# Optimization experiments

Hardware: AMD Instinct MI355X
Metric: run time of the kernel (lower is better)

The kernel has to match this reference:

```python
import jax, jax.numpy as jnp
import numpy as np
import math

D_MODEL = 1024
N_HEAD = 16


def setup_inputs() -> dict:
    key = jax.random.key(0)
    ks = jax.random.split(key, 11)
    B, S, D = 2, 2048, D_MODEL
    s = 1.0 / math.sqrt(D)
    return {
        "q": jax.random.normal(ks[0], (B, S, D), dtype=jnp.float32),
        "k": jax.random.normal(ks[1], (B, S, D), dtype=jnp.float32),
        "v": jax.random.normal(ks[2], (B, S, D), dtype=jnp.float32),
        "w_q": jax.random.normal(ks[3], (D, D), dtype=jnp.float32) * s,
        "b_q": jnp.zeros((D,), dtype=jnp.float32),
        "w_k": jax.random.normal(ks[4], (D, D), dtype=jnp.float32) * s,
        "b_k": jnp.zeros((D,), dtype=jnp.float32),
        "w_v": jax.random.normal(ks[5], (D, D), dtype=jnp.float32) * s,
        "b_v": jnp.zeros((D,), dtype=jnp.float32),
        "w_out": jax.random.normal(ks[6], (D, D), dtype=jnp.float32) * s,
        "b_out": jnp.zeros((D,), dtype=jnp.float32),
    }


def _split_heads(x, n_head):
    B, S, D = x.shape
    return x.reshape(B, S, n_head, D // n_head).transpose(0, 2, 1, 3)  # [B,H,S,dk]


def reference(q, k, v, w_q, b_q, w_k, b_k, w_v, b_v, w_out, b_out):
    # Linear projections (weights stored as [in, out])
    qh = _split_heads(q @ w_q + b_q, N_HEAD)
    kh = _split_heads(k @ w_k + b_k, N_HEAD)
    vh = _split_heads(v @ w_v + b_v, N_HEAD)
    d_k = qh.shape[-1]
    scores = jnp.einsum("bhqd,bhkd->bhqk", qh, kh) / jnp.sqrt(jnp.float32(d_k))
    attn = jax.nn.softmax(scores, axis=-1)
    context = jnp.einsum("bhqk,bhkd->bhqd", attn, vh)  # [B,H,S,dk]
    B, H, S, dk = context.shape
    context = context.transpose(0, 2, 1, 3).reshape(B, S, H * dk)
    return context @ w_out + b_out
```

## Files before the change

kernel.cpp:

```cpp
#include <hip/hip_runtime.h>
#include <hip/hip_bf16.h>


typedef __bf16 bf16x8 __attribute__((ext_vector_type(8)));
typedef float  f32x4  __attribute__((ext_vector_type(4)));

#define DEVI __device__ __forceinline__
#define SWZ(row, cb) ((cb) ^ (((row) & 7) << 4))

#define GLOAD16(gsrc, ldst)                                                    \
    __builtin_amdgcn_global_load_lds(                                          \
        (const __attribute__((address_space(1))) unsigned int*)(gsrc),         \
        (__attribute__((address_space(3))) unsigned int*)(ldst), 16, 0, 0)

#define BAR()        asm volatile("s_barrier" ::: "memory")
#define WAIT_LGKM0() asm volatile("s_waitcnt lgkmcnt(0)" ::: "memory")
#define WAIT_VM0()   asm volatile("s_waitcnt vmcnt(0)" ::: "memory")
#define WAIT_VM4()   asm volatile("s_waitcnt vmcnt(4)" ::: "memory")

static DEVI unsigned short f2bf(float f) {
    __hip_bfloat16 h = __float2bfloat16(f);
    return __builtin_bit_cast(unsigned short, h);
}
static DEVI unsigned int pack2(float a, float b) {
    return (unsigned int)f2bf(a) | ((unsigned int)f2bf(b) << 16);
}
static DEVI bf16x8 ldsRead(const char* p) {
    return __builtin_bit_cast(bf16x8, *(const uint4*)p);
}

__global__ __launch_bounds__(256) void wtrans_kernel(
    const float* w0, const float* w1, const float* w2, const float* w3,
    unsigned short* t0, unsigned short* t1, unsigned short* t2, unsigned short* t3)
{
    __shared__ unsigned short tile[64][80];
    const int z = blockIdx.z;
    const float* w = (z == 0) ? w0 : (z == 1) ? w1 : (z == 2) ? w2 : w3;
    unsigned short* wt = (z == 0) ? t0 : (z == 1) ? t1 : (z == 2) ? t2 : t3;
    const int n0 = blockIdx.x * 64, k0 = blockIdx.y * 64;
    const int t = threadIdx.x;
#pragma unroll
    for (int i = 0; i < 4; i++) {
        int chunk = t + i * 256;
        int row = chunk >> 4, c4 = chunk & 15;
        float4 v = *(const float4*)(w + (size_t)(k0 + row) * 1024 + n0 + c4 * 4);
        tile[c4 * 4 + 0][row] = f2bf(v.x);
        tile[c4 * 4 + 1][row] = f2bf(v.y);
        tile[c4 * 4 + 2][row] = f2bf(v.z);
        tile[c4 * 4 + 3][row] = f2bf(v.w);
    }
    __syncthreads();
#pragma unroll
    for (int i = 0; i < 2; i++) {
        int idx = t + i * 256;
        int row = idx >> 3, ch = idx & 7;
        uint4 vv = *(const uint4*)(&tile[row][ch * 8]);
        *(uint4*)(wt + (size_t)(n0 + row) * 1024 + k0 + ch * 8) = vv;
    }
}

__global__ __launch_bounds__(256, 3) void gemm_proj_kernel(
    const float* x0, const float* x1, const float* x2,
    const unsigned short* wt0, const unsigned short* wt1, const unsigned short* wt2,
    const float* b0, const float* b1, const float* b2,
    unsigned short* y0, unsigned short* y1, unsigned short* y2)
{
    __shared__ __align__(16) char Af[32768];
    __shared__ __align__(16) char Bs[16384];
    const int i = blockIdx.x;
    const int xcd = i & 7, j = i >> 3;
    const int panel = xcd * 12 + (j >> 3);
    const int z = panel >> 5, mblk = panel & 31;
    const int n0 = (j & 7) * 128, m0 = mblk * 128;

    const float* X = (z == 0) ? x0 : (z == 1) ? x1 : x2;
    const unsigned short* Wt = (z == 0) ? wt0 : (z == 1) ? wt1 : wt2;
    const float* bias = (z == 0) ? b0 : (z == 1) ? b1 : b2;
    unsigned short* Y = (z == 0) ? y0 : (z == 1) ? y1 : y2;
    const float scale = (z == 0) ? 0.125f * 1.44269504f : 1.0f;
    const int t = threadIdx.x, w = t >> 6, l = t & 63, l15 = l & 15, l4 = l >> 4;
    const int wr = w >> 1, wc = w & 1;
    const char* Ab = (const char*)X;
    const char* Bb = (const char*)Wt;

    f32x4 acc[4][4];
#pragma unroll
    for (int mr = 0; mr < 4; mr++)
#pragma unroll
        for (int nc = 0; nc < 4; nc++) acc[mr][nc] = f32x4{0.f, 0.f, 0.f, 0.f};

#pragma unroll 1
    for (int k = 0; k < 16; ++k) {
        const int k0 = k * 64;
        BAR();
#pragma unroll
        for (int jj = 0; jj < 8; jj++) {
            int o = w * 8192 + jj * 1024 + l * 16;
            int row = o >> 8, cb = (o >> 4) & 15;
            int csw = cb ^ ((row & 7) << 1);
            GLOAD16(Ab + ((size_t)(m0 + row) * 1024 + k0 + csw * 4) * 4,
                    Af + w * 8192 + jj * 1024);
        }
#pragma unroll
        for (int jj = 0; jj < 4; jj++) {
            int o = w * 4096 + jj * 1024 + l * 16;
            int row = o >> 7, cb = (o >> 4) & 7;
            int csw = cb ^ (row & 7);
            GLOAD16(Bb + ((size_t)(n0 + row) * 1024 + k0 + csw * 8) * 2,
                    Bs + w * 4096 + jj * 1024);
        }
        WAIT_VM0();
        BAR();

        bf16x8 af[4][2], bfr[4][2];
#pragma unroll
        for (int mr = 0; mr < 4; mr++) {
            int row = wr * 64 + mr * 16 + l15;
            int x = (row & 7) << 1;
#pragma unroll
            for (int kf = 0; kf < 2; kf++) {
                int cb = kf * 8 + l4 * 2;
                const char* p = Af + row * 256 + (cb ^ x) * 16;
                float4 a = *(const float4*)p;
                float4 b = *(const float4*)(p + 16);
                uint4 pk = {pack2(a.x, a.y), pack2(a.z, a.w),
                            pack2(b.x, b.y), pack2(b.z, b.w)};
                af[mr][kf] = __builtin_bit_cast(bf16x8, pk);
            }
        }
#pragma unroll
        for (int nc = 0; nc < 4; nc++) {
            int row = wc * 64 + nc * 16 + l15;
#pragma unroll
            for (int kf = 0; kf < 2; kf++)
                bfr[nc][kf] = ldsRead(Bs + row * 128 + SWZ(row, kf * 64 + l4 * 16));
        }
        __builtin_amdgcn_s_setprio(1);
#pragma unroll
        for (int kf = 0; kf < 2; kf++)
#pragma unroll
            for (int mr = 0; mr < 4; mr++)
#pragma unroll
                for (int nc = 0; nc < 4; nc++)
                    acc[mr][nc] = __builtin_amdgcn_mfma_f32_16x16x32_bf16(
                        af[mr][kf], bfr[nc][kf], acc[mr][nc], 0, 0, 0);
        __builtin_amdgcn_s_setprio(0);
    }

    WAIT_LGKM0();
    BAR();
    char* Es = Af;
    if (z < 2) {
#pragma unroll
        for (int nc = 0; nc < 4; nc++) {
            float bv = bias[n0 + wc * 64 + nc * 16 + l15];
#pragma unroll
            for (int mr = 0; mr < 4; mr++)
#pragma unroll
                for (int r = 0; r < 4; r++) {
                    int mloc = wr * 64 + mr * 16 + l4 * 4 + r;
                    int nloc = wc * 64 + nc * 16 + l15;
                    *(unsigned short*)(Es + mloc * 256 + nloc * 2) =
                        f2bf((acc[mr][nc][r] + bv) * scale);
                }
        }
        WAIT_LGKM0();
        BAR();
#pragma unroll
        for (int ii = 0; ii < 8; ii++) {
            int idx = t + ii * 256, row = idx >> 4, ch = idx & 15;
            *(uint4*)((char*)Y + ((size_t)(m0 + row) * 1024 + n0 + ch * 8) * 2) =
                *(const uint4*)(Es + row * 256 + ch * 16);
        }
    } else {
#pragma unroll
        for (int nc = 0; nc < 4; nc++) {
            float bv = bias[n0 + wc * 64 + nc * 16 + l15];
#pragma unroll
            for (int mr = 0; mr < 4; mr++)
#pragma unroll
                for (int r = 0; r < 4; r++) {
                    int mloc = wr * 64 + mr * 16 + l4 * 4 + r;
                    int nloc = wc * 64 + nc * 16 + l15;
                    *(unsigned short*)(Es + nloc * 256 + mloc * 2) =
                        f2bf(acc[mr][nc][r] + bv);
                }
        }
        WAIT_LGKM0();
        BAR();
        const int bb = m0 >> 11, s0 = m0 & 2047;
#pragma unroll
        for (int ii = 0; ii < 8; ii++) {
            int idx = t + ii * 256, row = idx >> 4, ch = idx & 15;
            int col = n0 + row, h = col >> 6, d = col & 63;
            *(uint4*)((char*)Y +
                      (((size_t)((bb * 16 + h) * 64 + d)) * 2048 + s0 + ch * 8) * 2) =
                *(const uint4*)(Es + row * 256 + ch * 16);
        }
    }
}

__global__ __launch_bounds__(256, 3) void attn_kernel(
    const unsigned short* Q2, const unsigned short* K2, const unsigned short* VT,
    unsigned short* ctx)
{
    __shared__ __align__(16) char sm[49152];
    char* QPs = sm;
    char* K0s = sm + 16384;
    char* K1s = sm + 24576;
    char* V0s = sm + 32768;
    char* V1s = sm + 40960;
    const int t = threadIdx.x, w = t >> 6, l = t & 63, l15 = l & 15, l4 = l >> 4;
    char* Ps = QPs + w * 4096;

    const int i = blockIdx.x;
    const int xcd = i & 7, j = i >> 3;
    const int bh = xcd * 4 + (j >> 4), qblk = j & 15;
    const int b = bh >> 4, h = bh & 15;
    const int q0 = qblk * 128;
    const int t0 = (qblk * 2) & 31;
    const char* Qb = (const char*)(Q2 + ((size_t)(b * 2048 + q0)) * 1024 + h * 64);
    const char* Kb = (const char*)(K2 + ((size_t)(b * 2048)) * 1024 + h * 64);
    const char* Vb = (const char*)(VT + (size_t)bh * 64 * 2048);

    int kGO[2], vGO[2];
#pragma unroll
    for (int jj = 0; jj < 2; jj++) {
        int row = w * 16 + jj * 8 + (l >> 3);
        int ch = (l & 7) ^ (row & 7);
        kGO[jj] = row * 2048 + ch * 16;
        vGO[jj] = row * 4096 + ch * 16;
    }
    int kRO[4][2];
#pragma unroll
    for (int cc = 0; cc < 4; cc++) {
        int row = cc * 16 + l15;
#pragma unroll
        for (int kf = 0; kf < 2; kf++)
            kRO[cc][kf] = row * 128 + SWZ(row, kf * 64 + l4 * 16);
    }
    int pWO[2][4], pRO[2][2];
#pragma unroll
    for (int qi = 0; qi < 2; qi++) {
        int row = qi * 16 + l15;
#pragma unroll
        for (int cc = 0; cc < 4; cc++) {
            int c = (cc * 2 + (l4 >> 1)) ^ (l15 & 7);
            pWO[qi][cc] = row * 128 + c * 16 + (l4 & 1) * 8;
        }
#pragma unroll
        for (int kf = 0; kf < 2; kf++)
            pRO[qi][kf] = row * 128 + SWZ(row, kf * 64 + l4 * 16);
    }

#define STAGE_KV(TT, Kdst, Vdst)                                               \
    do {                                                                       \
        int kk0 = (TT) * 64;                                                   \
        _Pragma("unroll") for (int jj = 0; jj < 2; jj++) {                     \
            GLOAD16(Kb + (size_t)(kk0 * 2048 + kGO[jj]),                       \
                    (Kdst) + w * 2048 + jj * 1024);                            \
            GLOAD16(Vb + (size_t)(kk0 * 2 + vGO[jj]),                          \
                    (Vdst) + w * 2048 + jj * 1024);                            \
        }                                                                      \
    } while (0)

    STAGE_KV(t0, K0s, V0s);

#pragma unroll
    for (int ii = 0; ii < 4; ii++) {
        int idx = t + ii * 256, row = idx >> 3, ch = idx & 7;
        uint4 vv = *(const uint4*)(Qb + (size_t)row * 2048 + ch * 16);
        *(uint4*)(QPs + row * 128 + SWZ(row, ch * 16)) = vv;
    }
    WAIT_LGKM0();
    BAR();
    bf16x8 qf[2][2];
#pragma unroll
    for (int qi = 0; qi < 2; qi++) {
        int row = w * 32 + qi * 16 + l15;
#pragma unroll
        for (int kf = 0; kf < 2; kf++)
            qf[qi][kf] = ldsRead(QPs + row * 128 + SWZ(row, kf * 64 + l4 * 16));
    }
    WAIT_LGKM0();
    BAR();

    bf16x8 ones;
#pragma unroll
    for (int e = 0; e < 8; e++) ones[e] = (__bf16)1.0f;

    f32x4 o[2][4], ol[2];
#pragma unroll
    for (int qi = 0; qi < 2; qi++) {
#pragma unroll
        for (int c = 0; c < 4; c++) o[qi][c] = f32x4{0.f, 0.f, 0.f, 0.f};
        ol[qi] = f32x4{0.f, 0.f, 0.f, 0.f};
    }

#pragma unroll 1
    for (int it = 0; it < 32; it++) {
        char* Kc = (it & 1) ? K1s : K0s;
        char* Vc = (it & 1) ? V1s : V0s;
        char* Kn = (it & 1) ? K0s : K1s;
        char* Vn = (it & 1) ? V0s : V1s;
        if (it < 31) {
            STAGE_KV((t0 + it + 1) & 31, Kn, Vn);
            WAIT_VM4();
        } else {
            WAIT_VM0();
        }
        BAR();

        f32x4 sacc[2][4];
#pragma unroll
        for (int qi = 0; qi < 2; qi++)
#pragma unroll
            for (int c = 0; c < 4; c++) sacc[qi][c] = f32x4{0.f, 0.f, 0.f, 0.f};
        __builtin_amdgcn_s_setprio(1);
#pragma unroll
        for (int cc = 0; cc < 4; cc++)
#pragma unroll
            for (int kf = 0; kf < 2; kf++) {
                bf16x8 kfrag = ldsRead(Kc + kRO[cc][kf]);
#pragma unroll
                for (int qi = 0; qi < 2; qi++)
                    sacc[qi][cc] = __builtin_amdgcn_mfma_f32_16x16x32_bf16(
                        kfrag, qf[qi][kf], sacc[qi][cc], 0, 0, 0);
            }
        __builtin_amdgcn_s_setprio(0);

#pragma unroll
        for (int qi = 0; qi < 2; qi++)
#pragma unroll
            for (int cc = 0; cc < 4; cc++)
#pragma unroll
                for (int r = 0; r < 4; r++) sacc[qi][cc][r] = exp2f(sacc[qi][cc][r]);

#pragma unroll
        for (int qi = 0; qi < 2; qi++)
#pragma unroll
            for (int cc = 0; cc < 4; cc++) {
                uint2 pk = {pack2(sacc[qi][cc][0], sacc[qi][cc][1]),
                            pack2(sacc[qi][cc][2], sacc[qi][cc][3])};
                *(uint2*)(Ps + pWO[qi][cc]) = pk;
            }
        asm volatile("" ::: "memory");
        bf16x8 pf[2][2];
#pragma unroll
        for (int qi = 0; qi < 2; qi++)
#pragma unroll
            for (int kf = 0; kf < 2; kf++)
                pf[qi][kf] = ldsRead(Ps + pRO[qi][kf]);

        __builtin_amdgcn_s_setprio(1);
#pragma unroll
        for (int dd = 0; dd < 4; dd++)
#pragma unroll
            for (int kf = 0; kf < 2; kf++) {
                bf16x8 vfrag = ldsRead(Vc + kRO[dd][kf]);
#pragma unroll
                for (int qi = 0; qi < 2; qi++)
                    o[qi][dd] = __builtin_amdgcn_mfma_f32_16x16x32_bf16(
                        vfrag, pf[qi][kf], o[qi][dd], 0, 0, 0);
            }
#pragma unroll
        for (int qi = 0; qi < 2; qi++)
#pragma unroll
            for (int kf = 0; kf < 2; kf++)
                ol[qi] = __builtin_amdgcn_mfma_f32_16x16x32_bf16(
                    ones, pf[qi][kf], ol[qi], 0, 0, 0);
        __builtin_amdgcn_s_setprio(0);

        WAIT_LGKM0();
        BAR();
    }
#undef STAGE_KV

#pragma unroll
    for (int qi = 0; qi < 2; qi++) {
        float rinv = 1.0f / ol[qi][0];
        int q = q0 + w * 32 + qi * 16 + l15;
        unsigned short* crow = ctx + ((size_t)(b * 2048 + q)) * 1024 + h * 64;
#pragma unroll
        for (int dd = 0; dd < 4; dd++) {
            uint2 pk = {pack2(o[qi][dd][0] * rinv, o[qi][dd][1] * rinv),
                        pack2(o[qi][dd][2] * rinv, o[qi][dd][3] * rinv)};
            *(uint2*)(crow + dd * 16 + l4 * 4) = pk;
        }
    }
}

__global__ __launch_bounds__(256, 3) void gemm_out_kernel(
    const unsigned short* ctx, const unsigned short* wto, const float* bias, float* out)
{
    __shared__ __align__(16) char As[16384];
    __shared__ __align__(16) char Bs[16384];
    const int i = blockIdx.x;
    const int xcd = i & 7, j = i >> 3;
    const int mpanel = xcd * 4 + (j >> 3);
    const int n0 = (j & 7) * 128, m0 = mpanel * 128;
    const int t = threadIdx.x, w = t >> 6, l = t & 63, l15 = l & 15, l4 = l >> 4;
    const int wr = w >> 1, wc = w & 1;
    const char* Ab = (const char*)ctx;
    const char* Bb = (const char*)wto;

    f32x4 acc[4][4];
#pragma unroll
    for (int mr = 0; mr < 4; mr++)
#pragma unroll
        for (int nc = 0; nc < 4; nc++) acc[mr][nc] = f32x4{0.f, 0.f, 0.f, 0.f};

#pragma unroll 1
    for (int k = 0; k < 16; ++k) {
        const int k0 = k * 64;
        BAR();
#pragma unroll
        for (int jj = 0; jj < 4; jj++) {
            int o = w * 4096 + jj * 1024 + l * 16;
            int row = o >> 7, cb = (o >> 4) & 7;
            int csw = cb ^ (row & 7);
            GLOAD16(Ab + ((size_t)(m0 + row) * 1024 + k0 + csw * 8) * 2,
                    As + w * 4096 + jj * 1024);
        }
#pragma unroll
        for (int jj = 0; jj < 4; jj++) {
            int o = w * 4096 + jj * 1024 + l * 16;
            int row = o >> 7, cb = (o >> 4) & 7;
            int csw = cb ^ (row & 7);
            GLOAD16(Bb + ((size_t)(n0 + row) * 1024 + k0 + csw * 8) * 2,
                    Bs + w * 4096 + jj * 1024);
        }
        WAIT_VM0();
        BAR();

        bf16x8 af[4][2], bfr[4][2];
#pragma unroll
        for (int mr = 0; mr < 4; mr++) {
            int row = wr * 64 + mr * 16 + l15;
#pragma unroll
            for (int kf = 0; kf < 2; kf++)
                af[mr][kf] = ldsRead(As + row * 128 + SWZ(row, kf * 64 + l4 * 16));
        }
#pragma unroll
        for (int nc = 0; nc < 4; nc++) {
            int row = wc * 64 + nc * 16 + l15;
#pragma unroll
            for (int kf = 0; kf < 2; kf++)
                bfr[nc][kf] = ldsRead(Bs + row * 128 + SWZ(row, kf * 64 + l4 * 16));
        }
        __builtin_amdgcn_s_setprio(1);
#pragma unroll
        for (int kf = 0; kf < 2; kf++)
#pragma unroll
            for (int mr = 0; mr < 4; mr++)
#pragma unroll
                for (int nc = 0; nc < 4; nc++)
                    acc[mr][nc] = __builtin_amdgcn_mfma_f32_16x16x32_bf16(
                        af[mr][kf], bfr[nc][kf], acc[mr][nc], 0, 0, 0);
        __builtin_amdgcn_s_setprio(0);
    }

#pragma unroll
    for (int nc = 0; nc < 4; nc++) {
        int col = n0 + wc * 64 + nc * 16 + l15;
        float bv = bias[col];
#pragma unroll
        for (int mr = 0; mr < 4; mr++)
#pragma unroll
            for (int r = 0; r < 4; r++) {
                int m = m0 + wr * 64 + mr * 16 + l4 * 4 + r;
                out[(size_t)m * 1024 + col] = acc[mr][nc][r] + bv;
            }
    }
}

extern "C" void kernel_launch(void* const* d_in, const int* in_sizes, int n_in,
                              void* d_out, int out_size, void* d_ws, size_t ws_size,
                              hipStream_t stream)
{
    (void)in_sizes; (void)n_in; (void)out_size; (void)ws_size;
    const float* q  = (const float*)d_in[0];
    const float* k  = (const float*)d_in[1];
    const float* v  = (const float*)d_in[2];
    const float* wq = (const float*)d_in[3];
    const float* bq = (const float*)d_in[4];
    const float* wk = (const float*)d_in[5];
    const float* bk = (const float*)d_in[6];
    const float* wv = (const float*)d_in[7];
    const float* bv = (const float*)d_in[8];
    const float* wo = (const float*)d_in[9];
    const float* bo = (const float*)d_in[10];

    char* ws = (char*)d_ws;
    const size_t MB = 1u << 20;
    unsigned short* WTq = (unsigned short*)(ws + 0 * MB);
    unsigned short* WTk = (unsigned short*)(ws + 2 * MB);
    unsigned short* WTv = (unsigned short*)(ws + 4 * MB);
    unsigned short* WTo = (unsigned short*)(ws + 6 * MB);
    unsigned short* Q2  = (unsigned short*)(ws + 8 * MB);
    unsigned short* K2  = (unsigned short*)(ws + 16 * MB);
    unsigned short* VT  = (unsigned short*)(ws + 24 * MB);
    unsigned short* CTX = (unsigned short*)(ws + 32 * MB);

    wtrans_kernel<<<dim3(16, 16, 4), 256, 0, stream>>>(wq, wk, wv, wo, WTq, WTk, WTv, WTo);
    gemm_proj_kernel<<<768, 256, 0, stream>>>(q, k, v, WTq, WTk, WTv,
                                              bq, bk, bv, Q2, K2, VT);
    attn_kernel<<<512, 256, 0, stream>>>(Q2, K2, VT, CTX);
    gemm_out_kernel<<<256, 256, 0, stream>>>(CTX, WTo, bo, (float*)d_out);
}
```

Baseline: 140.8 us.

## Split attention along keys into two halves and merge with a reduce kernel

Each attention block now processes half of the key range, doubling the grid to 1024 blocks. Partial unnormalized outputs go to a workspace in bf16 and row sums in fp32, and a new reduce kernel adds them and normalizes into ctx. The change also single-buffers V, loads Q straight into registers, and cuts LDS so four blocks fit per CU. The intent is better occupancy and load balance, at the cost of an extra kernel launch, extra global traffic for partials, and bf16 rounding of the partials before summation.

```diff
diff --git a/kernel.cpp b/kernel.cpp
--- a/kernel.cpp
+++ b/kernel.cpp
@@ -16,7 +16,7 @@
 #define BAR()        asm volatile("s_barrier" ::: "memory")
 #define WAIT_LGKM0() asm volatile("s_waitcnt lgkmcnt(0)" ::: "memory")
 #define WAIT_VM0()   asm volatile("s_waitcnt vmcnt(0)" ::: "memory")
-#define WAIT_VM4()   asm volatile("s_waitcnt vmcnt(4)" ::: "memory")
+#define WAIT_VM2()   asm volatile("s_waitcnt vmcnt(2)" ::: "memory")
 
 static DEVI unsigned short f2bf(float f) {
     __hip_bfloat16 h = __float2bfloat16(f);
@@ -24,6 +24,10 @@
 }
 static DEVI unsigned int pack2(float a, float b) {
     return (unsigned int)f2bf(a) | ((unsigned int)f2bf(b) << 16);
+}
+static DEVI float bf2f(unsigned int lo16) {
+    unsigned int x = lo16 << 16;
+    return __builtin_bit_cast(float, x);
 }
 static DEVI bf16x8 ldsRead(const char* p) {
     return __builtin_bit_cast(bf16x8, *(const uint4*)p);
@@ -200,36 +204,35 @@
     }
 }
 
-__global__ __launch_bounds__(256, 3) void attn_kernel(
+__global__ __launch_bounds__(256, 4) void attn_kernel(
     const unsigned short* Q2, const unsigned short* K2, const unsigned short* VT,
-    unsigned short* ctx)
+    unsigned short* Opart, float* lpart)
 {
-    __shared__ __align__(16) char sm[49152];
-    char* QPs = sm;
+    __shared__ __align__(16) char sm[40960];
+    char* Pall = sm;
     char* K0s = sm + 16384;
     char* K1s = sm + 24576;
-    char* V0s = sm + 32768;
-    char* V1s = sm + 40960;
+    char* Vs  = sm + 32768;
     const int t = threadIdx.x, w = t >> 6, l = t & 63, l15 = l & 15, l4 = l >> 4;
-    char* Ps = QPs + w * 4096;
+    char* Ps = Pall + w * 4096;
 
     const int i = blockIdx.x;
     const int xcd = i & 7, j = i >> 3;
-    const int bh = xcd * 4 + (j >> 4), qblk = j & 15;
+    const int bh = xcd * 4 + (j >> 5);
+    const int jj = j & 31, qblk = jj >> 1, kh = jj & 1;
     const int b = bh >> 4, h = bh & 15;
     const int q0 = qblk * 128;
-    const int t0 = (qblk * 2) & 31;
     const char* Qb = (const char*)(Q2 + ((size_t)(b * 2048 + q0)) * 1024 + h * 64);
     const char* Kb = (const char*)(K2 + ((size_t)(b * 2048)) * 1024 + h * 64);
     const char* Vb = (const char*)(VT + (size_t)bh * 64 * 2048);
 
     int kGO[2], vGO[2];
 #pragma unroll
-    for (int jj = 0; jj < 2; jj++) {
-        int row = w * 16 + jj * 8 + (l >> 3);
+    for (int jj2 = 0; jj2 < 2; jj2++) {
+        int row = w * 16 + jj2 * 8 + (l >> 3);
         int ch = (l & 7) ^ (row & 7);
-        kGO[jj] = row * 2048 + ch * 16;
-        vGO[jj] = row * 4096 + ch * 16;
+        kGO[jj2] = row * 2048 + ch * 16;
+        vGO[jj2] = row * 4096 + ch * 16;
     }
     int kRO[4][2];
 #pragma unroll
@@ -253,36 +256,35 @@
             pRO[qi][kf] = row * 128 + SWZ(row, kf * 64 + l4 * 16);
     }
 
-#define STAGE_KV(TT, Kdst, Vdst)                                               \
+#define STAGE_K(TT, Kdst)                                                      \
     do {                                                                       \
         int kk0 = (TT) * 64;                                                   \
-        _Pragma("unroll") for (int jj = 0; jj < 2; jj++) {                     \
-            GLOAD16(Kb + (size_t)(kk0 * 2048 + kGO[jj]),                       \
-                    (Kdst) + w * 2048 + jj * 1024);                            \
-            GLOAD16(Vb + (size_t)(kk0 * 2 + vGO[jj]),                          \
-                    (Vdst) + w * 2048 + jj * 1024);                            \
-        }                                                                      \
+        _Pragma("unroll") for (int s2 = 0; s2 < 2; s2++)                       \
+            GLOAD16(Kb + (size_t)(kk0 * 2048 + kGO[s2]),                       \
+                    (Kdst) + w * 2048 + s2 * 1024);                            \
     } while (0)
-
-    STAGE_KV(t0, K0s, V0s);
-
-#pragma unroll
-    for (int ii = 0; ii < 4; ii++) {
-        int idx = t + ii * 256, row = idx >> 3, ch = idx & 7;
-        uint4 vv = *(const uint4*)(Qb + (size_t)row * 2048 + ch * 16);
-        *(uint4*)(QPs + row * 128 + SWZ(row, ch * 16)) = vv;
-    }
-    WAIT_LGKM0();
-    BAR();
+#define STAGE_V(TT)                                                            \
+    do {                                                                       \
+        int kk0 = (TT) * 64;                                                   \
+        _Pragma("unroll") for (int s2 = 0; s2 < 2; s2++)                       \
+            GLOAD16(Vb + (size_t)(kk0 * 2 + vGO[s2]),                          \
+                    Vs + w * 2048 + s2 * 1024);                                \
+    } while (0)
+
     bf16x8 qf[2][2];
 #pragma unroll
     for (int qi = 0; qi < 2; qi++) {
         int row = w * 32 + qi * 16 + l15;
 #pragma unroll
         for (int kf = 0; kf < 2; kf++)
-            qf[qi][kf] = ldsRead(QPs + row * 128 + SWZ(row, kf * 64 + l4 * 16));
-    }
-    WAIT_LGKM0();
+            qf[qi][kf] = __builtin_bit_cast(
+                bf16x8, *(const uint4*)(Qb + (size_t)row * 2048 + kf * 64 + l4 * 16));
+    }
+
+    const int tbase = kh * 16;
+    STAGE_K(tbase + (qblk & 15), K0s);
+    STAGE_V(tbase + (qblk & 15));
+    WAIT_VM0();
     BAR();
 
     bf16x8 ones;
@@ -298,18 +300,10 @@
     }
 
 #pragma unroll 1
-    for (int it = 0; it < 32; it++) {
+    for (int it = 0; it < 16; it++) {
         char* Kc = (it & 1) ? K1s : K0s;
-        char* Vc = (it & 1) ? V1s : V0s;
         char* Kn = (it & 1) ? K0s : K1s;
-        char* Vn = (it & 1) ? V0s : V1s;
-        if (it < 31) {
-            STAGE_KV((t0 + it + 1) & 31, Kn, Vn);
-            WAIT_VM4();
-        } else {
-            WAIT_VM0();
-        }
-        BAR();
+        if (it < 15) STAGE_K(tbase + ((qblk + it + 1) & 15), Kn);
 
         f32x4 sacc[2][4];
 #pragma unroll
@@ -352,12 +346,15 @@
             for (int kf = 0; kf < 2; kf++)
                 pf[qi][kf] = ldsRead(Ps + pRO[qi][kf]);
 
+        if (it < 15) { WAIT_VM2(); } else { WAIT_VM0(); }
+        BAR();
+
         __builtin_amdgcn_s_setprio(1);
 #pragma unroll
         for (int dd = 0; dd < 4; dd++)
 #pragma unroll
             for (int kf = 0; kf < 2; kf++) {
-                bf16x8 vfrag = ldsRead(Vc + kRO[dd][kf]);
+                bf16x8 vfrag = ldsRead(Vs + kRO[dd][kf]);
 #pragma unroll
                 for (int qi = 0; qi < 2; qi++)
                     o[qi][dd] = __builtin_amdgcn_mfma_f32_16x16x32_bf16(
@@ -373,21 +370,50 @@
 
         WAIT_LGKM0();
         BAR();
-    }
-#undef STAGE_KV
-
+        if (it < 15) {
+            STAGE_V(tbase + ((qblk + it + 1) & 15));
+            WAIT_VM2();
+            BAR();
+        }
+    }
+#undef STAGE_K
+#undef STAGE_V
+
+    const size_t qgbase = (size_t)bh * 2048 + q0 + w * 32;
 #pragma unroll
     for (int qi = 0; qi < 2; qi++) {
-        float rinv = 1.0f / ol[qi][0];
-        int q = q0 + w * 32 + qi * 16 + l15;
-        unsigned short* crow = ctx + ((size_t)(b * 2048 + q)) * 1024 + h * 64;
+        size_t qg = qgbase + qi * 16 + l15;
+        unsigned short* orow = Opart + ((size_t)kh * 65536 + qg) * 64;
 #pragma unroll
         for (int dd = 0; dd < 4; dd++) {
-            uint2 pk = {pack2(o[qi][dd][0] * rinv, o[qi][dd][1] * rinv),
-                        pack2(o[qi][dd][2] * rinv, o[qi][dd][3] * rinv)};
-            *(uint2*)(crow + dd * 16 + l4 * 4) = pk;
-        }
-    }
+            uint2 pk = {pack2(o[qi][dd][0], o[qi][dd][1]),
+                        pack2(o[qi][dd][2], o[qi][dd][3])};
+            *(uint2*)(orow + dd * 16 + l4 * 4) = pk;
+        }
+        if (l4 == 0) lpart[(size_t)kh * 65536 + qg] = ol[qi][0];
+    }
+}
+
+__global__ __launch_bounds__(256) void reduce_kernel(
+    const unsigned short* Op, const float* lp, unsigned short* ctx)
+{
+    int idx = blockIdx.x * 256 + threadIdx.x;
+    int qg = idx >> 3, c8 = idx & 7;
+    uint4 a = *(const uint4*)(Op + (size_t)qg * 64 + c8 * 8);
+    uint4 bq = *(const uint4*)(Op + (size_t)65536 * 64 + (size_t)qg * 64 + c8 * 8);
+    float rinv = 1.0f / (lp[qg] + lp[65536 + qg]);
+    const unsigned int* pa = (const unsigned int*)&a;
+    const unsigned int* pb = (const unsigned int*)&bq;
+    unsigned int outp[4];
+#pragma unroll
+    for (int j = 0; j < 4; j++) {
+        float s0 = (bf2f(pa[j] & 0xffff) + bf2f(pb[j] & 0xffff)) * rinv;
+        float s1 = (bf2f(pa[j] >> 16) + bf2f(pb[j] >> 16)) * rinv;
+        outp[j] = pack2(s0, s1);
+    }
+    int bh = qg >> 11, s = qg & 2047, b = bh >> 4, h = bh & 15;
+    *(uint4*)(ctx + ((size_t)(b * 2048 + s)) * 1024 + h * 64 + c8 * 8) =
+        *(const uint4*)outp;
 }
 
 __global__ __launch_bounds__(256, 3) void gemm_out_kernel(
@@ -501,10 +527,13 @@
     unsigned short* K2  = (unsigned short*)(ws + 16 * MB);
     unsigned short* VT  = (unsigned short*)(ws + 24 * MB);
     unsigned short* CTX = (unsigned short*)(ws + 32 * MB);
+    unsigned short* OPART = (unsigned short*)(ws + 40 * MB);
+    float*          LPART = (float*)(ws + 57 * MB);
 
     wtrans_kernel<<<dim3(16, 16, 4), 256, 0, stream>>>(wq, wk, wv, wo, WTq, WTk, WTv, WTo);
     gemm_proj_kernel<<<768, 256, 0, stream>>>(q, k, v, WTq, WTk, WTv,
                                               bq, bk, bv, Q2, K2, VT);
-    attn_kernel<<<512, 256, 0, stream>>>(Q2, K2, VT, CTX);
+    attn_kernel<<<1024, 256, 0, stream>>>(Q2, K2, VT, OPART, LPART);
+    reduce_kernel<<<2048, 256, 0, stream>>>(OPART, LPART, CTX);
     gemm_out_kernel<<<256, 256, 0, stream>>>(CTX, WTo, bo, (float*)d_out);
 }
```

Result: no change. 142.1 us (+1.0%).
